# Kernel optimization log

Measured on AMD Instinct MI355X. Metric: run time of the kernel, lower is better.

Reference implementation:

```python
import jax, jax.numpy as jnp
import numpy as np

B, N, C, H = 2, 2048, 512, 8
D = C // H  # head dim = 64
SCALE = C ** -0.5  # module uses heads_channels**-0.5 (full inner dim, not per-head)


def setup_inputs() -> dict:
    key = jax.random.key(0)
    ks = jax.random.split(key, 9)
    return {
        "q": jax.random.normal(ks[0], (B, N, C), jnp.float32),
        "kv": jax.random.normal(ks[1], (B, N, C), jnp.float32),
        "pos_q": jax.random.normal(ks[2], (B, N, D), jnp.float32),
        "pos_k": jax.random.normal(ks[3], (B, N, D), jnp.float32),
        "Wq": jax.random.normal(ks[4], (C, C), jnp.float32) * (C ** -0.5),
        "Wk": jax.random.normal(ks[5], (C, C), jnp.float32) * (C ** -0.5),
        "Wv": jax.random.normal(ks[6], (C, C), jnp.float32) * (C ** -0.5),
        "Wo": jax.random.normal(ks[7], (C, C), jnp.float32) * (C ** -0.5),
        "bo": jnp.zeros((C,), jnp.float32),
    }


def reference(q, kv, pos_q, pos_k, Wq, Wk, Wv, Wo, bo):
    # projections: [b n c] @ [c c] -> [b n c]
    qp = q @ Wq
    kp = kv @ Wk
    vp = kv @ Wv
    # split heads: b n (h d) -> b h n d
    split = lambda t: t.reshape(B, N, H, D).transpose(0, 2, 1, 3)
    qh, kh, vh = split(qp), split(kp), split(vp)
    # additive positional bias, broadcast over heads: b n d -> b 1 n d
    qh = qh + pos_q[:, None, :, :]
    kh = kh + pos_k[:, None, :, :]
    sim = jnp.einsum("bhid,bhjd->bhij", qh, kh) * SCALE
    attn = jax.nn.softmax(sim, axis=-1)
    out = jnp.einsum("bhij,bhjd->bhid", attn, vh)
    # merge heads: b h n d -> b n (h d)
    out = out.transpose(0, 2, 1, 3).reshape(B, N, C)
    return out @ Wo + bo
```

## Files before the change

### kernel.cpp

```cpp
#include <hip/hip_runtime.h>
#include <hip/hip_bf16.h>
#include <stdint.h>
#include <math.h>

static constexpr int kB = 2, kN = 2048, kC = 512, kH = 8, kD = 64;
static constexpr float kScaleL2E =
    (float)(0.044194173824159216 * 1.4426950408889634);
static constexpr int kSplit = 2;
static constexpr size_t kSegF = (size_t)kB * kN * kC;

typedef short bf16x8 __attribute__((ext_vector_type(8)));
typedef short bf16x4 __attribute__((ext_vector_type(4)));
typedef float f32x4  __attribute__((ext_vector_type(4)));

__device__ __forceinline__ float bf2f(unsigned short u) {
  union { unsigned int i; float f; } v; v.i = ((unsigned int)u) << 16; return v.f;
}
__device__ __forceinline__ unsigned short f2bf(float f) {
  union { float f; unsigned int i; } v; v.f = f;
  unsigned int x = v.i;
  return (unsigned short)((x + 0x7FFFu + ((x >> 16) & 1u)) >> 16);
}
__device__ __forceinline__ short f2bs(float f) { return (short)f2bf(f); }
__device__ __forceinline__ unsigned int pack2_t(float lo, float hi) {
  union { float f; unsigned int i; } a, b; a.f = lo; b.f = hi;
  return (b.i & 0xFFFF0000u) | (a.i >> 16);
}
__device__ __forceinline__ float fast_exp2(float x) {
#if __has_builtin(__builtin_amdgcn_exp2f)
  return __builtin_amdgcn_exp2f(x);
#else
  return exp2f(x);
#endif
}

__device__ __forceinline__ int vcol(int k) {
  return 32 * (k >> 5) + ((k >> 2) & 3) * 8 + ((k >> 4) & 1) * 4;
}

__global__ __launch_bounds__(256) void prep_kernel(
    const float* __restrict__ q, const float* __restrict__ kv,
    const float* __restrict__ Wq, const float* __restrict__ Wk,
    const float* __restrict__ Wv,
    unsigned short* __restrict__ qbf, unsigned short* __restrict__ kvbf,
    unsigned short* __restrict__ wT)
{
  const int t = threadIdx.x;
  if (blockIdx.z == 0) {
    const int gid = blockIdx.x * 256 + t;
    #pragma unroll
    for (int it = 0; it < 8; ++it) {
      int i4 = gid + it * 65536;
      float4 a = *(const float4*)(q + (size_t)i4 * 4);
      float4 b = *(const float4*)(kv + (size_t)i4 * 4);
      bf16x4 ab = {f2bs(a.x), f2bs(a.y), f2bs(a.z), f2bs(a.w)};
      bf16x4 bb = {f2bs(b.x), f2bs(b.y), f2bs(b.z), f2bs(b.w)};
      *(bf16x4*)(qbf + (size_t)i4 * 4) = ab;
      *(bf16x4*)(kvbf + (size_t)i4 * 4) = bb;
    }
  } else {
    if (blockIdx.x >= 192) return;
    const int wsel = blockIdx.x >> 6;
    const int tile = blockIdx.x & 63;
    const int tr = tile >> 3, tc = tile & 7;
    const float* W = (wsel == 0) ? Wq : (wsel == 1 ? Wk : Wv);
    unsigned short* out = wT + (size_t)wsel * kC * kC;

    __shared__ __align__(16) float Ts[64][68];
    #pragma unroll
    for (int it = 0; it < 4; ++it) {
      int e = t + it * 256;
      int r = e >> 4, c4 = (e & 15) * 4;
      *(float4*)&Ts[r][c4] =
          *(const float4*)(W + (size_t)(tr * 64 + r) * kC + tc * 64 + c4);
    }
    __syncthreads();
    const int n = t >> 2, ks = (t & 3) * 16;
    unsigned short* orow = out + (size_t)(tc * 64 + n) * kC + tr * 64 + ks;
    #pragma unroll
    for (int c = 0; c < 4; ++c) {
      ushort4 o;
      o.x = f2bf(Ts[ks + c * 4 + 0][n]);
      o.y = f2bf(Ts[ks + c * 4 + 1][n]);
      o.z = f2bf(Ts[ks + c * 4 + 2][n]);
      o.w = f2bf(Ts[ks + c * 4 + 3][n]);
      *(ushort4*)(orow + c * 4) = o;
    }
  }
}

__global__ __launch_bounds__(256) void proj_kernel(
    const unsigned short* __restrict__ qbf,
    const unsigned short* __restrict__ kvbf,
    const unsigned short* __restrict__ wT,
    const float* __restrict__ pos_q,
    const float* __restrict__ pos_k,
    unsigned short* __restrict__ qh,
    unsigned short* __restrict__ kh,
    unsigned short* __restrict__ vhT)
{
  const bool kvmode = (blockIdx.z == 1);
  const unsigned short* A = kvmode ? kvbf : qbf;
  const unsigned short* Bt0 = wT + (kvmode ? (size_t)kC * kC : 0);
  const unsigned short* Bt1 = wT + 2 * (size_t)kC * kC;

  __shared__ __align__(16) unsigned short As[128][72];
  __shared__ __align__(16) unsigned short Bs[2][64][72];

  const int t = threadIdx.x;
  const int w = t >> 6, lane = t & 63;
  const int l15 = lane & 15, quad = lane >> 4;
  const int m0 = blockIdx.x * 128;
  const int n0 = blockIdx.y * 64;

  const int sr = t >> 3, sc = (t & 7) * 8;

  bf16x8 pa[4], pb0[2], pb1[2];
  #pragma unroll
  for (int i = 0; i < 4; ++i)
    pa[i] = *(const bf16x8*)(A + (size_t)(m0 + sr + i * 32) * kC + sc);
  #pragma unroll
  for (int i = 0; i < 2; ++i)
    pb0[i] = *(const bf16x8*)(Bt0 + (size_t)(n0 + sr + i * 32) * kC + sc);
  if (kvmode)
    #pragma unroll
    for (int i = 0; i < 2; ++i)
      pb1[i] = *(const bf16x8*)(Bt1 + (size_t)(n0 + sr + i * 32) * kC + sc);

  f32x4 acc0[2][4], acc1[2][4];
  #pragma unroll
  for (int si = 0; si < 2; ++si)
    #pragma unroll
    for (int ct = 0; ct < 4; ++ct) {
      acc0[si][ct] = (f32x4){0.f, 0.f, 0.f, 0.f};
      acc1[si][ct] = (f32x4){0.f, 0.f, 0.f, 0.f};
    }

  for (int k0 = 0; k0 < kC; k0 += 64) {
    if (k0) __syncthreads();
    #pragma unroll
    for (int i = 0; i < 4; ++i) *(bf16x8*)&As[sr + i * 32][sc] = pa[i];
    #pragma unroll
    for (int i = 0; i < 2; ++i) *(bf16x8*)&Bs[0][sr + i * 32][sc] = pb0[i];
    if (kvmode)
      #pragma unroll
      for (int i = 0; i < 2; ++i) *(bf16x8*)&Bs[1][sr + i * 32][sc] = pb1[i];
    __syncthreads();
    if (k0 + 64 < kC) {
      int kn = k0 + 64;
      #pragma unroll
      for (int i = 0; i < 4; ++i)
        pa[i] = *(const bf16x8*)(A + (size_t)(m0 + sr + i * 32) * kC + kn + sc);
      #pragma unroll
      for (int i = 0; i < 2; ++i)
        pb0[i] = *(const bf16x8*)(Bt0 + (size_t)(n0 + sr + i * 32) * kC + kn + sc);
      if (kvmode)
        #pragma unroll
        for (int i = 0; i < 2; ++i)
          pb1[i] = *(const bf16x8*)(Bt1 + (size_t)(n0 + sr + i * 32) * kC + kn + sc);
    }
    bf16x8 a0[2], a1[2];
    #pragma unroll
    for (int si = 0; si < 2; ++si) {
      a0[si] = *(const bf16x8*)&As[w * 32 + si * 16 + l15][quad * 8];
      a1[si] = *(const bf16x8*)&As[w * 32 + si * 16 + l15][32 + quad * 8];
    }
    #pragma unroll
    for (int ct = 0; ct < 4; ++ct) {
      bf16x8 b0 = *(const bf16x8*)&Bs[0][ct * 16 + l15][quad * 8];
      bf16x8 b1 = *(const bf16x8*)&Bs[0][ct * 16 + l15][32 + quad * 8];
      #pragma unroll
      for (int si = 0; si < 2; ++si) {
        acc0[si][ct] = __builtin_amdgcn_mfma_f32_16x16x32_bf16(a0[si], b0, acc0[si][ct], 0, 0, 0);
        acc0[si][ct] = __builtin_amdgcn_mfma_f32_16x16x32_bf16(a1[si], b1, acc0[si][ct], 0, 0, 0);
      }
      if (kvmode) {
        bf16x8 c0 = *(const bf16x8*)&Bs[1][ct * 16 + l15][quad * 8];
        bf16x8 c1 = *(const bf16x8*)&Bs[1][ct * 16 + l15][32 + quad * 8];
        #pragma unroll
        for (int si = 0; si < 2; ++si) {
          acc1[si][ct] = __builtin_amdgcn_mfma_f32_16x16x32_bf16(a0[si], c0, acc1[si][ct], 0, 0, 0);
          acc1[si][ct] = __builtin_amdgcn_mfma_f32_16x16x32_bf16(a1[si], c1, acc1[si][ct], 0, 0, 0);
        }
      }
    }
  }

  const int h = n0 >> 6;
  if (!kvmode) {
    #pragma unroll
    for (int si = 0; si < 2; ++si)
      #pragma unroll
      for (int r = 0; r < 4; ++r) {
        int m = m0 + w * 32 + si * 16 + quad * 4 + r;
        int b = m >> 11, n_seq = m & (kN - 1);
        #pragma unroll
        for (int ct = 0; ct < 4; ++ct) {
          int d = ct * 16 + l15;
          float val = (acc0[si][ct][r] +
                       pos_q[((size_t)b * kN + n_seq) * kD + d]) * kScaleL2E;
          qh[(((size_t)b * kH + h) * kN + n_seq) * kD + d] = f2bf(val);
        }
      }
  } else {
    #pragma unroll
    for (int si = 0; si < 2; ++si)
      #pragma unroll
      for (int r = 0; r < 4; ++r) {
        int m = m0 + w * 32 + si * 16 + quad * 4 + r;
        int b = m >> 11, n_seq = m & (kN - 1);
        #pragma unroll
        for (int ct = 0; ct < 4; ++ct) {
          int d = ct * 16 + l15;
          float vk = acc0[si][ct][r] + pos_k[((size_t)b * kN + n_seq) * kD + d];
          kh[(((size_t)b * kH + h) * kN + n_seq) * kD + d] = f2bf(vk);
        }
      }
    __syncthreads();
    unsigned short (*Tv)[136] = (unsigned short(*)[136])&As[0][0];
    #pragma unroll
    for (int si = 0; si < 2; ++si)
      #pragma unroll
      for (int ct = 0; ct < 4; ++ct) {
        const int d = ct * 16 + l15;
        const int nl = w * 32 + si * 16 + quad * 4;
        unsigned int lo = (unsigned int)f2bf(acc1[si][ct][0]) |
                          ((unsigned int)f2bf(acc1[si][ct][1]) << 16);
        unsigned int hi = (unsigned int)f2bf(acc1[si][ct][2]) |
                          ((unsigned int)f2bf(acc1[si][ct][3]) << 16);
        *(unsigned int*)&Tv[d][nl]     = lo;
        *(unsigned int*)&Tv[d][nl + 2] = hi;
      }
    __syncthreads();
    const int c16 = t & 15, dr = t >> 4;
    const int b2 = m0 >> 11, nbase = m0 & (kN - 1);
    #pragma unroll
    for (int rep = 0; rep < 4; ++rep) {
      const int d = rep * 16 + dr;
      bf16x8 vv = *(const bf16x8*)&Tv[d][c16 * 8];
      *(bf16x8*)(vhT + (((size_t)(b2 * kH + h)) * kD + d) * kN + nbase + c16 * 8) = vv;
    }
  }
}

__global__ __launch_bounds__(256, 8) void attn_kernel(
    const unsigned short* __restrict__ qh,
    const unsigned short* __restrict__ kh,
    const unsigned short* __restrict__ vhT,
    unsigned short* __restrict__ opart,
    float* __restrict__ lbuf)
{
  const int sid = (blockIdx.x & 7) * 128 + (blockIdx.x >> 3);
  const int s  = sid >> 9;
  const int bh = (sid >> 5) & 15;
  const int q0 = (sid & 31) * 64;
  const int b = bh >> 3, h = bh & 7;
  const int kbase = s * (kN / kSplit);
  const int nkt = kN / kSplit / 64;
  const int t = threadIdx.x;
  const int w = t >> 6, lane = t & 63;
  const int l15 = lane & 15, quad = lane >> 4;

  __shared__ __align__(16) unsigned short Kb_s[64][72];
  __shared__ __align__(16) unsigned short Vt_s[64][72];

  const unsigned short* Qb = qh  + (size_t)bh * kN * kD;
  const unsigned short* Kb = kh  + (size_t)bh * kN * kD;
  const unsigned short* Vb = vhT + (size_t)bh * kD * kN;

  bf16x8 aq0, aq1;
  {
    const unsigned short* qrow = Qb + (size_t)(q0 + w * 16 + l15) * kD;
    aq0 = *(const bf16x8*)(qrow + quad * 8);
    aq1 = *(const bf16x8*)(qrow + 32 + quad * 8);
  }

  const int sr = t >> 3, sc = (t & 7) * 8, sr2 = sr + 32;
  const int vc1 = vcol(sc), vc2 = vcol(sc + 4);

  const unsigned short* pK0 = Kb + (size_t)(kbase + sr) * kD + sc;
  const unsigned short* pK1 = Kb + (size_t)(kbase + sr2) * kD + sc;
  const unsigned short* pV0 = Vb + (size_t)sr * kN + kbase + sc;
  const unsigned short* pV1 = Vb + (size_t)sr2 * kN + kbase + sc;
  const size_t kStepK = (size_t)64 * kD;

  bf16x8 pk0 = *(const bf16x8*)pK0;
  bf16x8 pk1 = *(const bf16x8*)pK1;
  bf16x8 pv0 = *(const bf16x8*)pV0;
  bf16x8 pv1 = *(const bf16x8*)pV1;

  f32x4 o[4];
  #pragma unroll
  for (int nt = 0; nt < 4; ++nt) o[nt] = (f32x4){0.f, 0.f, 0.f, 0.f};
  float l_run = 0.f;

  for (int i = 0; i < nkt; ++i) {
    __syncthreads();
    *(bf16x8*)&Kb_s[sr][sc]  = pk0;
    *(bf16x8*)&Kb_s[sr2][sc] = pk1;
    {
      bf16x4 lo0 = {pv0[0], pv0[1], pv0[2], pv0[3]};
      bf16x4 hi0 = {pv0[4], pv0[5], pv0[6], pv0[7]};
      bf16x4 lo1 = {pv1[0], pv1[1], pv1[2], pv1[3]};
      bf16x4 hi1 = {pv1[4], pv1[5], pv1[6], pv1[7]};
      *(bf16x4*)&Vt_s[sr][vc1]  = lo0;
      *(bf16x4*)&Vt_s[sr][vc2]  = hi0;
      *(bf16x4*)&Vt_s[sr2][vc1] = lo1;
      *(bf16x4*)&Vt_s[sr2][vc2] = hi1;
    }
    __syncthreads();

    f32x4 sacc[4];
    __builtin_amdgcn_s_setprio(1);
    #pragma unroll
    for (int ct = 0; ct < 4; ++ct) {
      bf16x8 ak0 = *(const bf16x8*)&Kb_s[ct * 16 + l15][quad * 8];
      bf16x8 ak1 = *(const bf16x8*)&Kb_s[ct * 16 + l15][32 + quad * 8];
      f32x4 zz = (f32x4){0.f, 0.f, 0.f, 0.f};
      zz = __builtin_amdgcn_mfma_f32_16x16x32_bf16(ak0, aq0, zz, 0, 0, 0);
      zz = __builtin_amdgcn_mfma_f32_16x16x32_bf16(ak1, aq1, zz, 0, 0, 0);
      sacc[ct] = zz;
    }
    __builtin_amdgcn_s_setprio(0);

    if (i + 1 < nkt) {
      pK0 += kStepK; pK1 += kStepK;
      pk0 = *(const bf16x8*)pK0;
      pk1 = *(const bf16x8*)pK1;
    }

    union PB8 { unsigned int u[4]; bf16x8 v; } pb01, pb23;
    {
      float psum = 0.f;
      #pragma unroll
      for (int ct = 0; ct < 4; ++ct)
        #pragma unroll
        for (int r = 0; r < 4; ++r) {
          float p = fast_exp2(sacc[ct][r]);
          sacc[ct][r] = p;
          psum += p;
        }
      l_run += psum;
      pb01.u[0] = pack2_t(sacc[0][0], sacc[0][1]);
      pb01.u[1] = pack2_t(sacc[0][2], sacc[0][3]);
      pb01.u[2] = pack2_t(sacc[1][0], sacc[1][1]);
      pb01.u[3] = pack2_t(sacc[1][2], sacc[1][3]);
      pb23.u[0] = pack2_t(sacc[2][0], sacc[2][1]);
      pb23.u[1] = pack2_t(sacc[2][2], sacc[2][3]);
      pb23.u[2] = pack2_t(sacc[3][0], sacc[3][1]);
      pb23.u[3] = pack2_t(sacc[3][2], sacc[3][3]);
    }

    if (i + 1 < nkt) {
      pV0 += 64; pV1 += 64;
      pv0 = *(const bf16x8*)pV0;
      pv1 = *(const bf16x8*)pV1;
    }

    __builtin_amdgcn_s_setprio(1);
    #pragma unroll
    for (int nt = 0; nt < 4; ++nt) {
      bf16x8 av0 = *(const bf16x8*)&Vt_s[nt * 16 + l15][quad * 8];
      bf16x8 av1 = *(const bf16x8*)&Vt_s[nt * 16 + l15][32 + quad * 8];
      o[nt] = __builtin_amdgcn_mfma_f32_16x16x32_bf16(av0, pb01.v, o[nt], 0, 0, 0);
      o[nt] = __builtin_amdgcn_mfma_f32_16x16x32_bf16(av1, pb23.v, o[nt], 0, 0, 0);
    }
    __builtin_amdgcn_s_setprio(0);
  }

  l_run += __shfl_xor(l_run, 16);
  l_run += __shfl_xor(l_run, 32);
  if (quad == 0)
    lbuf[(size_t)(s * 16 + bh) * kN + q0 + w * 16 + l15] = l_run;

  __syncthreads();
  unsigned short (*Ot)[72] = (unsigned short(*)[72])&Kb_s[0][0];
  {
    const int ql = w * 16 + l15;
    #pragma unroll
    for (int nt = 0; nt < 4; ++nt) {
      unsigned int lo = (unsigned int)f2bf(o[nt][0]) |
                        ((unsigned int)f2bf(o[nt][1]) << 16);
      unsigned int hi = (unsigned int)f2bf(o[nt][2]) |
                        ((unsigned int)f2bf(o[nt][3]) << 16);
      const int d0 = nt * 16 + quad * 4;
      *(unsigned int*)&Ot[ql][d0]     = lo;
      *(unsigned int*)&Ot[ql][d0 + 2] = hi;
    }
  }
  __syncthreads();
  {
    unsigned short* od = opart + (size_t)s * kSegF;
    const int c8 = t & 7, qb = t >> 3;
    #pragma unroll
    for (int rep = 0; rep < 2; ++rep) {
      const int ql = rep * 32 + qb;
      bf16x8 vv = *(const bf16x8*)&Ot[ql][c8 * 8];
      *(bf16x8*)(od + ((size_t)b * kN + (q0 + ql)) * kC + h * kD + c8 * 8) = vv;
    }
  }
}

__global__ __launch_bounds__(256) void proj_out_kernel(
    const unsigned short* __restrict__ opart,
    const float* __restrict__ lbuf,
    const float* __restrict__ Wo,
    const float* __restrict__ bo,
    float* __restrict__ out)
{
  __shared__ __align__(16) unsigned short Wt[64][72];

  const int t = threadIdx.x;
  const int w = t >> 6, lane = t & 63;
  const int l15 = lane & 15, quad = lane >> 4;
  const int m0 = blockIdx.x * 64;
  const int n0 = blockIdx.y * 64;

  const int m = m0 + w * 16 + l15;
  const int nseq = m & (kN - 1);
  const int bb = m >> 11;
  const size_t arow = (size_t)m * kC;

  ushort4 pw[4];
  #pragma unroll
  for (int i = 0; i < 4; ++i) {
    int e = t + i * 256;
    int r = e >> 4, c4 = (e & 15) * 4;
    float4 wv = *(const float4*)(Wo + (size_t)r * kC + n0 + c4);
    pw[i] = make_ushort4(f2bf(wv.x), f2bf(wv.y), f2bf(wv.z), f2bf(wv.w));
  }

  f32x4 acc[4];
  #pragma unroll
  for (int ct = 0; ct < 4; ++ct) acc[ct] = (f32x4){0.f, 0.f, 0.f, 0.f};

  #pragma unroll
  for (int k0 = 0; k0 < kC; k0 += 64) {
    if (k0) __syncthreads();
    #pragma unroll
    for (int i = 0; i < 4; ++i) {
      int e = t + i * 256;
      int r = e >> 4, c4 = (e & 15) * 4;
      Wt[c4 + 0][r] = pw[i].x;
      Wt[c4 + 1][r] = pw[i].y;
      Wt[c4 + 2][r] = pw[i].z;
      Wt[c4 + 3][r] = pw[i].w;
    }
    __syncthreads();

    const int h = k0 >> 6;
    const int bh = bb * 8 + h;
    float lsum = 0.f;
    #pragma unroll
    for (int s = 0; s < kSplit; ++s)
      lsum += lbuf[(size_t)(s * 16 + bh) * kN + nseq];
    const float wgt = 1.f / lsum;

    float af0[8] = {}, af1[8] = {};
    #pragma unroll
    for (int s = 0; s < kSplit; ++s) {
      bf16x8 v0 = *(const bf16x8*)(opart + (size_t)s * kSegF + arow + k0 + quad * 8);
      bf16x8 v1 = *(const bf16x8*)(opart + (size_t)s * kSegF + arow + k0 + 32 + quad * 8);
      #pragma unroll
      for (int j = 0; j < 8; ++j) {
        af0[j] += bf2f((unsigned short)v0[j]);
        af1[j] += bf2f((unsigned short)v1[j]);
      }
    }
    bf16x8 a0, a1;
    #pragma unroll
    for (int j = 0; j < 8; ++j) {
      a0[j] = (short)f2bf(af0[j] * wgt);
      a1[j] = (short)f2bf(af1[j] * wgt);
    }

    if (k0 + 64 < kC) {
      int kn = k0 + 64;
      #pragma unroll
      for (int i = 0; i < 4; ++i) {
        int e = t + i * 256;
        int r = e >> 4, c4 = (e & 15) * 4;
        float4 wv = *(const float4*)(Wo + (size_t)(kn + r) * kC + n0 + c4);
        pw[i] = make_ushort4(f2bf(wv.x), f2bf(wv.y), f2bf(wv.z), f2bf(wv.w));
      }
    }
    #pragma unroll
    for (int ct = 0; ct < 4; ++ct) {
      bf16x8 b0 = *(const bf16x8*)&Wt[ct * 16 + l15][quad * 8];
      bf16x8 b1 = *(const bf16x8*)&Wt[ct * 16 + l15][32 + quad * 8];
      acc[ct] = __builtin_amdgcn_mfma_f32_16x16x32_bf16(a0, b0, acc[ct], 0, 0, 0);
      acc[ct] = __builtin_amdgcn_mfma_f32_16x16x32_bf16(a1, b1, acc[ct], 0, 0, 0);
    }
  }

  #pragma unroll
  for (int ct = 0; ct < 4; ++ct) {
    int n = n0 + ct * 16 + l15;
    float bb2 = bo[n];
    #pragma unroll
    for (int r = 0; r < 4; ++r) {
      int mm = m0 + w * 16 + quad * 4 + r;
      out[(size_t)mm * kC + n] = acc[ct][r] + bb2;
    }
  }
}

extern "C" void kernel_launch(void* const* d_in, const int* in_sizes, int n_in,
                              void* d_out, int out_size, void* d_ws, size_t ws_size,
                              hipStream_t stream) {
  (void)in_sizes; (void)n_in; (void)out_size; (void)ws_size;
  const float* q     = (const float*)d_in[0];
  const float* kv    = (const float*)d_in[1];
  const float* pos_q = (const float*)d_in[2];
  const float* pos_k = (const float*)d_in[3];
  const float* Wq    = (const float*)d_in[4];
  const float* Wk    = (const float*)d_in[5];
  const float* Wv    = (const float*)d_in[6];
  const float* Wo    = (const float*)d_in[7];
  const float* bo    = (const float*)d_in[8];
  float* out = (float*)d_out;

  const size_t seg = (size_t)kB * kH * kN * kD;

  unsigned short* qbf  = (unsigned short*)d_ws;
  unsigned short* kvbf = qbf + seg;
  unsigned short* wT   = kvbf + seg;
  unsigned short* qhp  = wT + 3 * (size_t)kC * kC;
  unsigned short* khp  = qhp + seg;
  unsigned short* vtp  = khp + seg;
  unsigned short* opart = vtp + seg;
  float* lbuf = (float*)(opart + (size_t)kSplit * kSegF);

  dim3 blk(256);
  prep_kernel<<<dim3(256, 1, 2), blk, 0, stream>>>(q, kv, Wq, Wk, Wv, qbf, kvbf, wT);
  proj_kernel<<<dim3(32, 8, 2), blk, 0, stream>>>(qbf, kvbf, wT, pos_q, pos_k,
                                                  qhp, khp, vtp);
  attn_kernel<<<dim3(1024), blk, 0, stream>>>(qhp, khp, vtp, opart, lbuf);
  proj_out_kernel<<<dim3(64, 8), blk, 0, stream>>>(opart, lbuf, Wo, bo, out);
}
```

Measured before the change: 142.8 us.

## Double-buffer K/V shared tiles to drop one barrier per iteration

Shared-memory K and V tiles are double-buffered. The first tile is staged before the loop, and each iteration computes from one buffer while writing the next prefetched tile into the other after the PV MMAs. This removes the second __syncthreads per key tile, so the store-to-LDS no longer sits between barriers and the compute. In exchange the kernel's LDS footprint doubles, which likely lowers how many blocks fit per CU compared with the previous 8-block launch bound.

Measured after the change: 141.4 us. Within noise of the previous version (-0.9%).

```diff
diff --git a/kernel.cpp b/kernel.cpp
--- a/kernel.cpp
+++ b/kernel.cpp
@@ -261,8 +261,8 @@
   const int w = t >> 6, lane = t & 63;
   const int l15 = lane & 15, quad = lane >> 4;
 
-  __shared__ __align__(16) unsigned short Kb_s[64][72];
-  __shared__ __align__(16) unsigned short Vt_s[64][72];
+  __shared__ __align__(16) unsigned short Kb_s[2][64][72];
+  __shared__ __align__(16) unsigned short Vt_s[2][64][72];
 
   const unsigned short* Qb = qh  + (size_t)bh * kN * kD;
   const unsigned short* Kb = kh  + (size_t)bh * kN * kD;
@@ -284,6 +284,23 @@
   const unsigned short* pV1 = Vb + (size_t)sr2 * kN + kbase + sc;
   const size_t kStepK = (size_t)64 * kD;
 
+  {
+    bf16x8 k0v = *(const bf16x8*)pK0;
+    bf16x8 k1v = *(const bf16x8*)pK1;
+    bf16x8 v0v = *(const bf16x8*)pV0;
+    bf16x8 v1v = *(const bf16x8*)pV1;
+    *(bf16x8*)&Kb_s[0][sr][sc]  = k0v;
+    *(bf16x8*)&Kb_s[0][sr2][sc] = k1v;
+    bf16x4 lo0 = {v0v[0], v0v[1], v0v[2], v0v[3]};
+    bf16x4 hi0 = {v0v[4], v0v[5], v0v[6], v0v[7]};
+    bf16x4 lo1 = {v1v[0], v1v[1], v1v[2], v1v[3]};
+    bf16x4 hi1 = {v1v[4], v1v[5], v1v[6], v1v[7]};
+    *(bf16x4*)&Vt_s[0][sr][vc1]  = lo0;
+    *(bf16x4*)&Vt_s[0][sr][vc2]  = hi0;
+    *(bf16x4*)&Vt_s[0][sr2][vc1] = lo1;
+    *(bf16x4*)&Vt_s[0][sr2][vc2] = hi1;
+  }
+  pK0 += kStepK; pK1 += kStepK; pV0 += 64; pV1 += 64;
   bf16x8 pk0 = *(const bf16x8*)pK0;
   bf16x8 pk1 = *(const bf16x8*)pK1;
   bf16x8 pv0 = *(const bf16x8*)pV0;
@@ -296,38 +313,21 @@
 
   for (int i = 0; i < nkt; ++i) {
     __syncthreads();
-    *(bf16x8*)&Kb_s[sr][sc]  = pk0;
-    *(bf16x8*)&Kb_s[sr2][sc] = pk1;
-    {
-      bf16x4 lo0 = {pv0[0], pv0[1], pv0[2], pv0[3]};
-      bf16x4 hi0 = {pv0[4], pv0[5], pv0[6], pv0[7]};
-      bf16x4 lo1 = {pv1[0], pv1[1], pv1[2], pv1[3]};
-      bf16x4 hi1 = {pv1[4], pv1[5], pv1[6], pv1[7]};
-      *(bf16x4*)&Vt_s[sr][vc1]  = lo0;
-      *(bf16x4*)&Vt_s[sr][vc2]  = hi0;
-      *(bf16x4*)&Vt_s[sr2][vc1] = lo1;
-      *(bf16x4*)&Vt_s[sr2][vc2] = hi1;
-    }
-    __syncthreads();
+    const unsigned short (*Kr)[72] = Kb_s[i & 1];
+    const unsigned short (*Vr)[72] = Vt_s[i & 1];
 
     f32x4 sacc[4];
     __builtin_amdgcn_s_setprio(1);
     #pragma unroll
     for (int ct = 0; ct < 4; ++ct) {
-      bf16x8 ak0 = *(const bf16x8*)&Kb_s[ct * 16 + l15][quad * 8];
-      bf16x8 ak1 = *(const bf16x8*)&Kb_s[ct * 16 + l15][32 + quad * 8];
+      bf16x8 ak0 = *(const bf16x8*)&Kr[ct * 16 + l15][quad * 8];
+      bf16x8 ak1 = *(const bf16x8*)&Kr[ct * 16 + l15][32 + quad * 8];
       f32x4 zz = (f32x4){0.f, 0.f, 0.f, 0.f};
       zz = __builtin_amdgcn_mfma_f32_16x16x32_bf16(ak0, aq0, zz, 0, 0, 0);
       zz = __builtin_amdgcn_mfma_f32_16x16x32_bf16(ak1, aq1, zz, 0, 0, 0);
       sacc[ct] = zz;
     }
     __builtin_amdgcn_s_setprio(0);
-
-    if (i + 1 < nkt) {
-      pK0 += kStepK; pK1 += kStepK;
-      pk0 = *(const bf16x8*)pK0;
-      pk1 = *(const bf16x8*)pK1;
-    }
 
     union PB8 { unsigned int u[4]; bf16x8 v; } pb01, pb23;
     {
@@ -351,21 +351,37 @@
       pb23.u[3] = pack2_t(sacc[3][2], sacc[3][3]);
     }
 
-    if (i + 1 < nkt) {
-      pV0 += 64; pV1 += 64;
-      pv0 = *(const bf16x8*)pV0;
-      pv1 = *(const bf16x8*)pV1;
-    }
-
     __builtin_amdgcn_s_setprio(1);
     #pragma unroll
     for (int nt = 0; nt < 4; ++nt) {
-      bf16x8 av0 = *(const bf16x8*)&Vt_s[nt * 16 + l15][quad * 8];
-      bf16x8 av1 = *(const bf16x8*)&Vt_s[nt * 16 + l15][32 + quad * 8];
+      bf16x8 av0 = *(const bf16x8*)&Vr[nt * 16 + l15][quad * 8];
+      bf16x8 av1 = *(const bf16x8*)&Vr[nt * 16 + l15][32 + quad * 8];
       o[nt] = __builtin_amdgcn_mfma_f32_16x16x32_bf16(av0, pb01.v, o[nt], 0, 0, 0);
       o[nt] = __builtin_amdgcn_mfma_f32_16x16x32_bf16(av1, pb23.v, o[nt], 0, 0, 0);
     }
     __builtin_amdgcn_s_setprio(0);
+
+    if (i + 1 < nkt) {
+      unsigned short (*Kw)[72] = Kb_s[(i + 1) & 1];
+      unsigned short (*Vw)[72] = Vt_s[(i + 1) & 1];
+      *(bf16x8*)&Kw[sr][sc]  = pk0;
+      *(bf16x8*)&Kw[sr2][sc] = pk1;
+      bf16x4 lo0 = {pv0[0], pv0[1], pv0[2], pv0[3]};
+      bf16x4 hi0 = {pv0[4], pv0[5], pv0[6], pv0[7]};
+      bf16x4 lo1 = {pv1[0], pv1[1], pv1[2], pv1[3]};
+      bf16x4 hi1 = {pv1[4], pv1[5], pv1[6], pv1[7]};
+      *(bf16x4*)&Vw[sr][vc1]  = lo0;
+      *(bf16x4*)&Vw[sr][vc2]  = hi0;
+      *(bf16x4*)&Vw[sr2][vc1] = lo1;
+      *(bf16x4*)&Vw[sr2][vc2] = hi1;
+      if (i + 2 < nkt) {
+        pK0 += kStepK; pK1 += kStepK; pV0 += 64; pV1 += 64;
+        pk0 = *(const bf16x8*)pK0;
+        pk1 = *(const bf16x8*)pK1;
+        pv0 = *(const bf16x8*)pV0;
+        pv1 = *(const bf16x8*)pV1;
+      }
+    }
   }
 
   l_run += __shfl_xor(l_run, 16);
@@ -374,7 +390,7 @@
     lbuf[(size_t)(s * 16 + bh) * kN + q0 + w * 16 + l15] = l_run;
 
   __syncthreads();
-  unsigned short (*Ot)[72] = (unsigned short(*)[72])&Kb_s[0][0];
+  unsigned short (*Ot)[72] = (unsigned short(*)[72])&Kb_s[0][0][0];
   {
     const int ql = w * 16 + l15;
     #pragma unroll
```
